# Performance work log

Measured on AMD Instinct MI355X. Metric: run time of the kernel, lower is better.

The kernel has to match this reference:

```python
import jax, jax.numpy as jnp
import numpy as np

B, T, R, E, H = 64, 512, 256, 512, 1024

def setup_inputs() -> dict:
    key = jax.random.key(0)
    ks = jax.random.split(key, 7)
    s = lambda d: 1.0 / np.sqrt(d)
    return {
        "x": jax.random.normal(ks[0], (B, T, R), jnp.float32),
        "W_emb": jax.random.normal(ks[1], (E, R), jnp.float32) * s(R),
        "b_emb": jax.random.normal(ks[2], (E,), jnp.float32) * s(R),
        "W_ih": jax.random.normal(ks[3], (4 * H, E), jnp.float32) * s(H),
        "W_hh": jax.random.normal(ks[4], (4 * H, H), jnp.float32) * s(H),
        "b_ih": jax.random.normal(ks[5], (4 * H,), jnp.float32) * s(H),
        "b_hh": jax.random.normal(ks[6], (4 * H,), jnp.float32) * s(H),
    }

def reference(x, W_emb, b_emb, W_ih, W_hh, b_ih, b_hh):
    # Per-timestep Linear embedding, batched over time (same math as the loop)
    xe = jnp.einsum('btr,er->bte', x, W_emb) + b_emb            # [B,T,E]
    # Input contribution to all gates, precomputed for every step
    gx = jnp.einsum('bte,ge->btg', xe, W_ih) + (b_ih + b_hh)    # [B,T,4H]

    def step(carry, gx_t):
        h, c = carry
        gates = gx_t + h @ W_hh.T                               # [B,4H]
        i, f, g, o = jnp.split(gates, 4, axis=-1)
        i = jax.nn.sigmoid(i)
        f = jax.nn.sigmoid(f)
        g = jnp.tanh(g)
        o = jax.nn.sigmoid(o)
        c_new = f * c + i * g
        h_new = o * jnp.tanh(c_new)
        return (h_new, c_new), h_new

    h0 = jnp.zeros((x.shape[0], H), x.dtype)
    c0 = jnp.zeros((x.shape[0], H), x.dtype)
    (h_t, c_t), ys = jax.lax.scan(step, (h0, c0), jnp.swapaxes(gx, 0, 1))
    outputs = jnp.swapaxes(ys, 0, 1)                            # [B,T,H]
    return outputs, h_t, c_t
```

## Files before the change

### kernel.cpp

```cpp
#include <hip/hip_runtime.h>
#include <stdint.h>

typedef __attribute__((ext_vector_type(8))) short short8;
typedef __attribute__((ext_vector_type(4))) float f32x4;
typedef __attribute__((ext_vector_type(4))) unsigned short ushort4v;
typedef unsigned long long u64;

__device__ inline unsigned short f2bf(float x) {
  union { float f; unsigned u; } v; v.f = x;
  unsigned r = (v.u + 0x7FFFu + ((v.u >> 16) & 1u)) >> 16;
  return (unsigned short)r;
}
__device__ inline float bf2f(unsigned short b) {
  union { unsigned u; float f; } v; v.u = ((unsigned)b) << 16;
  return v.f;
}
__device__ inline float fsig(float x) { return 1.f / (1.f + __expf(-x)); }

__device__ inline void gload_lds16(const void* g, void* l) {
  __builtin_amdgcn_global_load_lds(
      (const __attribute__((address_space(1))) unsigned int*)g,
      (__attribute__((address_space(3))) unsigned int*)l, 16, 0, 0);
}

__global__ void k_convert(const float* __restrict__ src, unsigned short* __restrict__ dst, int n4) {
  int i = blockIdx.x * blockDim.x + threadIdx.x;
  if (i < n4) {
    f32x4 v = *(const f32x4*)(src + (size_t)i * 4);
    ushort4v r;
    r.x = f2bf(v.x); r.y = f2bf(v.y); r.z = f2bf(v.z); r.w = f2bf(v.w);
    *(ushort4v*)(dst + (size_t)i * 4) = r;
  }
}

__global__ void k_bias(const float* __restrict__ a, const float* __restrict__ b,
                       float* __restrict__ o, int n) {
  int i = blockIdx.x * blockDim.x + threadIdx.x;
  if (i < n) o[i] = a[i] + b[i];
}

__global__ void k_init(unsigned short* __restrict__ h0, unsigned short* __restrict__ flags) {
  int i = blockIdx.x * blockDim.x + threadIdx.x;
  h0[i] = 0;
  if (i < 256) flags[i] = 0;
}

template <int MODE>
__global__ __launch_bounds__(256) void k_gemm_bt(
    const unsigned short* __restrict__ A,
    const unsigned short* __restrict__ Bm,
    const float* __restrict__ bias,
    unsigned short* __restrict__ C,
    int M, int N, int K) {
  __shared__ unsigned short As[128 * 32];
  __shared__ unsigned short Bs[128 * 32];
  const int tid = threadIdx.x;

  int bidx = blockIdx.x, bidy = blockIdx.y;
  if (MODE == 1) {
    int bid = blockIdx.y * gridDim.x + blockIdx.x;
    int cpx = (gridDim.x * gridDim.y) >> 3;
    int swz = (bid & 7) * cpx + (bid >> 3);
    bidy = swz / gridDim.x;
    bidx = swz % gridDim.x;
  }
  const int m0 = bidy * 128, n0 = bidx * 128;
  const int lane = tid & 63, w = tid >> 6;
  const int wm = (w >> 1) * 64, wn = (w & 1) * 64;

  f32x4 acc[4][4] = {};

  const int ar0 = tid >> 2;
  const int ak = (tid & 3) * 8;
  const unsigned short* Ag0 = A + (size_t)(m0 + ar0) * K + ak;
  const unsigned short* Ag1 = A + (size_t)(m0 + 64 + ar0) * K + ak;
  const unsigned short* Bg0 = Bm + (size_t)(n0 + ar0) * K + ak;
  const unsigned short* Bg1 = Bm + (size_t)(n0 + 64 + ar0) * K + ak;
  unsigned short* Al = As + tid * 8;
  unsigned short* Bl = Bs + tid * 8;

  const int lr = lane & 15, lk = (lane >> 4) * 8;

  for (int k0 = 0; k0 < K; k0 += 32) {
    gload_lds16(Ag0 + k0, Al);
    gload_lds16(Ag1 + k0, Al + 2048);
    gload_lds16(Bg0 + k0, Bl);
    gload_lds16(Bg1 + k0, Bl + 2048);
    __syncthreads();
    short8 a[4], b[4];
#pragma unroll
    for (int i = 0; i < 4; i++) a[i] = *(const short8*)&As[(wm + i * 16 + lr) * 32 + lk];
#pragma unroll
    for (int j = 0; j < 4; j++) b[j] = *(const short8*)&Bs[(wn + j * 16 + lr) * 32 + lk];
#pragma unroll
    for (int i = 0; i < 4; i++)
#pragma unroll
      for (int j = 0; j < 4; j++)
        acc[i][j] = __builtin_amdgcn_mfma_f32_16x16x32_bf16(a[i], b[j], acc[i][j], 0, 0, 0);
    __syncthreads();
  }

  const int lq = (lane >> 4) * 4;
#pragma unroll
  for (int j = 0; j < 4; j++) {
    int col = n0 + wn + j * 16 + lr;
    float bv = bias[col];
#pragma unroll
    for (int i = 0; i < 4; i++) {
      int rowb = m0 + wm + i * 16 + lq;
#pragma unroll
      for (int r = 0; r < 4; r++) {
        int row = rowb + r;
        float v = acc[i][j][r] + bv;
        if (MODE == 1) {
          int t = row & 511, bglob = row >> 9;
          int gg = bglob >> 4, bb = bglob & 15;
          int s = col >> 10, cc = col & 1023;
          int gtb = cc >> 4, cl = cc & 15;
          int wv = cl >> 2, qq = cl & 3;
          size_t idx = (size_t)t * 262144 + (size_t)gg * 65536 + (size_t)gtb * 1024
                     + (size_t)((wv * 64 + bb * 4 + qq) * 4 + s);
          C[idx] = f2bf(v);
        } else {
          C[(size_t)row * (size_t)N + col] = f2bf(v);
        }
      }
    }
  }
}

#define R32(F) F(0) F(1) F(2) F(3) F(4) F(5) F(6) F(7) \
               F(8) F(9) F(10) F(11) F(12) F(13) F(14) F(15) \
               F(16) F(17) F(18) F(19) F(20) F(21) F(22) F(23) \
               F(24) F(25) F(26) F(27) F(28) F(29) F(30) F(31)
#define WDECL(i) short8 w##i;
#define WLOAD(i) asm volatile("global_load_dwordx4 %0, %1, off offset:%c2" \
                              : "=v"(w##i) : "v"(wbase), "i"((i) * 64));
#define MFH(i, ACC) { \
    short8 a_ = *(const short8*)(HsB + lB + (i) * 1024); \
    ACC = __builtin_amdgcn_mfma_f32_16x16x32_bf16(a_, w##i, ACC, 0, 0, 0); }
#define MF2(i, ACC) { \
    union { u64 d[2]; short8 s; } u_; \
    u_.d[0] = __hip_atomic_load((const u64*)(hrow2 + (i) * 32), __ATOMIC_RELAXED, __HIP_MEMORY_SCOPE_AGENT); \
    u_.d[1] = __hip_atomic_load((const u64*)(hrow2 + (i) * 32 + 4), __ATOMIC_RELAXED, __HIP_MEMORY_SCOPE_AGENT); \
    ACC = __builtin_amdgcn_mfma_f32_16x16x32_bf16(u_.s, w##i, ACC, 0, 0, 0); }

template <int RING>
__global__ __launch_bounds__(256, 1) void k_persist(
    const unsigned short* __restrict__ gx3,
    const unsigned short* __restrict__ Whh,
    unsigned short* __restrict__ hring,
    unsigned short* __restrict__ flags,
    float* __restrict__ out,
    float* __restrict__ hout,
    float* __restrict__ cout) {
  __shared__ unsigned short Hs[16384];
  __shared__ float Gs[4][16 * 17 + 4];

  const int tid = threadIdx.x;
  const int g = blockIdx.x & 3, gt = blockIdx.x >> 2;
  const int lane = tid & 63, w = tid >> 6;
  const int lr = lane & 15, hi = lane >> 4;

  const int grow = (lr >> 2) * 1024 + gt * 16 + w * 4 + (lr & 3);
  const unsigned short* wbase = Whh + (size_t)grow * 1024 + hi * 8;
  R32(WDECL)
  R32(WLOAD)
  asm volatile("s_waitcnt vmcnt(0)" ::: "memory");
  __builtin_amdgcn_sched_barrier(0);

  const int cb = lane >> 2, cq = lane & 3;
  const int col = gt * 16 + w * 4 + cq;
  const int brow = g * 16 + cb;
  float c_reg = 0.f;

  const u64* gbase = (const u64*)gx3 + (size_t)g * 16384 + (size_t)gt * 256;
  u64 gv = gbase[tid];

  const char* HsB = (const char*)Hs;
  const int lB = hi * 256 + lr * 16;

  const u64* fpw = (const u64*)flags + g * 16 + w * 4 + (lane & 3);

  for (int t = 0; t < 512; ++t) {
    f32x4 ac0 = {}, ac1 = {}, ac2 = {}, ac3 = {};
    if (RING == 2) {
      if (w == 0) {
        const u64* fp = (const u64*)flags + g * 16 + lane;
        for (;;) {
          bool ok = true;
          if (lane < 16) {
            u64 f = __hip_atomic_load(fp, __ATOMIC_RELAXED, __HIP_MEMORY_SCOPE_AGENT);
            ok = ((int)(f & 0xFFFF) >= t) && ((int)((f >> 16) & 0xFFFF) >= t) &&
                 ((int)((f >> 32) & 0xFFFF) >= t) && ((int)(f >> 48) >= t);
          }
          if (__all(ok)) break;
        }
      }
      __syncthreads();
      __builtin_amdgcn_sched_barrier(0);
      const unsigned short* hrow2 = hring + (size_t)(t & 1) * 65536
                                  + (size_t)(g * 16 + lr) * 1024 + hi * 8;
      MF2(0, ac0)  MF2(1, ac1)  MF2(2, ac2)  MF2(3, ac3)
      MF2(4, ac0)  MF2(5, ac1)  MF2(6, ac2)  MF2(7, ac3)
      MF2(8, ac0)  MF2(9, ac1)  MF2(10, ac2) MF2(11, ac3)
      MF2(12, ac0) MF2(13, ac1) MF2(14, ac2) MF2(15, ac3)
      MF2(16, ac0) MF2(17, ac1) MF2(18, ac2) MF2(19, ac3)
      MF2(20, ac0) MF2(21, ac1) MF2(22, ac2) MF2(23, ac3)
      MF2(24, ac0) MF2(25, ac1) MF2(26, ac2) MF2(27, ac3)
      MF2(28, ac0) MF2(29, ac1) MF2(30, ac2) MF2(31, ac3)
    } else {
      for (;;) {
        u64 f = __hip_atomic_load(fpw, __ATOMIC_RELAXED, __HIP_MEMORY_SCOPE_AGENT);
        bool ok = ((int)(f & 0xFFFF) >= t) && ((int)((f >> 16) & 0xFFFF) >= t) &&
                  ((int)((f >> 32) & 0xFFFF) >= t) && ((int)(f >> 48) >= t);
        if (__all(ok)) break;
      }
      __builtin_amdgcn_sched_barrier(0);
      const unsigned short* hsrc = hring + (size_t)t * 65536 + (size_t)g * 16384;
#pragma unroll
      for (int i = 0; i < 8; ++i) {
        int ch = w * 512 + i * 64;
        gload_lds16(hsrc + ((size_t)ch + lane) * 8, Hs + (size_t)ch * 8);
      }
      asm volatile("s_waitcnt vmcnt(0)" ::: "memory");
      __builtin_amdgcn_sched_barrier(0);
      __syncthreads();
      MFH(0, ac0)  MFH(1, ac1)  MFH(2, ac2)  MFH(3, ac3)
      MFH(4, ac0)  MFH(5, ac1)  MFH(6, ac2)  MFH(7, ac3)
      MFH(8, ac0)  MFH(9, ac1)  MFH(10, ac2) MFH(11, ac3)
      MFH(12, ac0) MFH(13, ac1) MFH(14, ac2) MFH(15, ac3)
      MFH(16, ac0) MFH(17, ac1) MFH(18, ac2) MFH(19, ac3)
      MFH(20, ac0) MFH(21, ac1) MFH(22, ac2) MFH(23, ac3)
      MFH(24, ac0) MFH(25, ac1) MFH(26, ac2) MFH(27, ac3)
      MFH(28, ac0) MFH(29, ac1) MFH(30, ac2) MFH(31, ac3)
    }
    f32x4 accs = (ac0 + ac1) + (ac2 + ac3);

#pragma unroll
    for (int r = 0; r < 4; ++r)
      Gs[w][(hi * 4 + r) * 17 + lr] = accs[r];
    asm volatile("s_waitcnt lgkmcnt(0)" ::: "memory");
    __builtin_amdgcn_sched_barrier(0);

    float gi = Gs[w][cb * 17 + 0 + cq]  + bf2f((unsigned short)(gv));
    float gf = Gs[w][cb * 17 + 4 + cq]  + bf2f((unsigned short)(gv >> 16));
    float gg = Gs[w][cb * 17 + 8 + cq]  + bf2f((unsigned short)(gv >> 32));
    float go = Gs[w][cb * 17 + 12 + cq] + bf2f((unsigned short)(gv >> 48));
    float i_ = fsig(gi);
    float f_ = fsig(gf);
    float g_ = tanhf(gg);
    float o_ = fsig(go);
    float cn = f_ * c_reg + i_ * g_;
    float hn = o_ * tanhf(cn);
    c_reg = cn;

    if (t == 511) {
      __builtin_nontemporal_store(hn, &out[((size_t)brow * 512 + t) * 1024 + col]);
      hout[(size_t)brow * 1024 + col] = hn;
      cout[(size_t)brow * 1024 + col] = cn;
    } else {
      unsigned hu = f2bf(hn);
      unsigned v0 = __shfl(hu, (lane & ~3) + 0);
      unsigned v1 = __shfl(hu, (lane & ~3) + 1);
      unsigned v2 = __shfl(hu, (lane & ~3) + 2);
      unsigned v3 = __shfl(hu, (lane & ~3) + 3);
      if ((lane & 3) == 0) {
        u64 pack = (u64)(v0 & 0xFFFF) | ((u64)(v1 & 0xFFFF) << 16)
                 | ((u64)(v2 & 0xFFFF) << 32) | ((u64)(v3 & 0xFFFF) << 48);
        u64* hp;
        if (RING == 2) {
          hp = (u64*)(hring + (size_t)((t + 1) & 1) * 65536
                      + (size_t)brow * 1024 + gt * 16 + w * 4);
        } else {
          size_t e = (size_t)(gt * 2 + (w >> 1)) * 128 + (size_t)cb * 8 + (size_t)(w & 1) * 4;
          hp = (u64*)(hring + (size_t)(t + 1) * 65536 + (size_t)g * 16384 + e);
        }
        __hip_atomic_store(hp, pack, __ATOMIC_RELAXED, __HIP_MEMORY_SCOPE_AGENT);
      }
      __syncthreads();
      if (tid == 0)
        __hip_atomic_store(&flags[g * 64 + gt], (unsigned short)(t + 1),
                           __ATOMIC_RELAXED, __HIP_MEMORY_SCOPE_AGENT);
      __builtin_nontemporal_store(hn, &out[((size_t)brow * 512 + t) * 1024 + col]);
      gv = gbase[(size_t)(t + 1) * 65536 + tid];
    }
  }
}
#undef MF2
#undef MFH
#undef WLOAD
#undef WDECL
#undef R32

extern "C" void kernel_launch(void* const* d_in, const int* in_sizes, int n_in,
                              void* d_out, int out_size, void* d_ws, size_t ws_size,
                              hipStream_t stream) {
  const float* x = (const float*)d_in[0];
  const float* W_emb = (const float*)d_in[1];
  const float* b_emb = (const float*)d_in[2];
  const float* W_ih = (const float*)d_in[3];
  const float* W_hh = (const float*)d_in[4];
  const float* b_ih = (const float*)d_in[5];
  const float* b_hh = (const float*)d_in[6];

  char* ws = (char*)d_ws;
  unsigned short* x_bf    = (unsigned short*)(ws + 0);
  unsigned short* Wemb_bf = (unsigned short*)(ws + 16777216);
  unsigned short* Wih_bf  = (unsigned short*)(ws + 17039360);
  unsigned short* Whh_bf  = (unsigned short*)(ws + 21233664);
  float* bias_sum         = (float*)(ws + 29622272);
  unsigned short* xe      = (unsigned short*)(ws + 29638656);
  unsigned short* gx3     = (unsigned short*)(ws + 63193088);
  unsigned short* flags   = (unsigned short*)(ws + 331628544);
  unsigned short* hring   = (unsigned short*)(ws + 331632640);

  const size_t need_ring = 331632640ull + 512ull * 131072ull;
  const bool big = (ws_size >= need_ring);

  float* out = (float*)d_out;
  float* hout = out + (size_t)64 * 512 * 1024;
  float* cout = hout + 65536;

  k_convert<<<8192, 256, 0, stream>>>(x, x_bf, 2097152);
  k_convert<<<128, 256, 0, stream>>>(W_emb, Wemb_bf, 32768);
  k_convert<<<2048, 256, 0, stream>>>(W_ih, Wih_bf, 524288);
  k_convert<<<4096, 256, 0, stream>>>(W_hh, Whh_bf, 1048576);
  k_bias<<<16, 256, 0, stream>>>(b_ih, b_hh, bias_sum, 4096);
  k_init<<<256, 256, 0, stream>>>(hring, flags);

  k_gemm_bt<0><<<dim3(4, 256), 256, 0, stream>>>(x_bf, Wemb_bf, b_emb, xe, 32768, 512, 256);
  k_gemm_bt<1><<<dim3(32, 256), 256, 0, stream>>>(xe, Wih_bf, bias_sum, gx3, 32768, 4096, 512);

  if (big)
    k_persist<512><<<256, 256, 0, stream>>>(gx3, Whh_bf, hring, flags, out, hout, cout);
  else
    k_persist<2><<<256, 256, 0, stream>>>(gx3, Whh_bf, hring, flags, out, hout, cout);
}
```

Before: 2.144 ms.

## Fold embedding weights into input-gate weights to skip the xe GEMM

Precomputes W_comb = W_ih·W_emb (4096x256) and a combined bias W_ih·b_emb + b_ih + b_hh, so the gate pre-activations come from a single GEMM over x with K=256. This removes the large [B*T,512] embedding GEMM and its intermediate write/read, and halves K for the big gate GEMM. In exchange it adds a small weight-weight GEMM, a transpose kernel and a serial bias dot-product kernel. Rounding the combined weight to bf16 changes numerics slightly.

```diff
diff --git a/kernel.cpp b/kernel.cpp
--- a/kernel.cpp
+++ b/kernel.cpp
@@ -33,16 +33,27 @@
   }
 }
 
-__global__ void k_bias(const float* __restrict__ a, const float* __restrict__ b,
-                       float* __restrict__ o, int n) {
-  int i = blockIdx.x * blockDim.x + threadIdx.x;
-  if (i < n) o[i] = a[i] + b[i];
-}
-
-__global__ void k_init(unsigned short* __restrict__ h0, unsigned short* __restrict__ flags) {
+__global__ void k_temb(const float* __restrict__ We, unsigned short* __restrict__ WT) {
+  int o = blockIdx.x * blockDim.x + threadIdx.x;
+  int r = o >> 9, e = o & 511;
+  WT[o] = f2bf(We[e * 256 + r]);
+}
+
+__global__ void k_bcomb(const float* __restrict__ Wih, const float* __restrict__ b_emb,
+                        const float* __restrict__ b_ih, const float* __restrict__ b_hh,
+                        float* __restrict__ out) {
+  int g = blockIdx.x * blockDim.x + threadIdx.x;
+  const float* row = Wih + (size_t)g * 512;
+  float s = 0.f;
+  for (int e = 0; e < 512; ++e) s += row[e] * b_emb[e];
+  out[g] = s + b_ih[g] + b_hh[g];
+}
+
+__global__ void k_init(unsigned short* __restrict__ h0, unsigned short* __restrict__ flags,
+                       float* __restrict__ zerob) {
   int i = blockIdx.x * blockDim.x + threadIdx.x;
   h0[i] = 0;
-  if (i < 256) flags[i] = 0;
+  if (i < 256) { flags[i] = 0; zerob[i] = 0.f; }
 }
 
 template <int MODE>
@@ -306,11 +317,12 @@
 
   char* ws = (char*)d_ws;
   unsigned short* x_bf    = (unsigned short*)(ws + 0);
-  unsigned short* Wemb_bf = (unsigned short*)(ws + 16777216);
+  unsigned short* WembT   = (unsigned short*)(ws + 16777216);
   unsigned short* Wih_bf  = (unsigned short*)(ws + 17039360);
   unsigned short* Whh_bf  = (unsigned short*)(ws + 21233664);
-  float* bias_sum         = (float*)(ws + 29622272);
-  unsigned short* xe      = (unsigned short*)(ws + 29638656);
+  float* b_comb           = (float*)(ws + 29622272);
+  float* zerob            = (float*)(ws + 29638656);
+  unsigned short* Wcomb   = (unsigned short*)(ws + 29639680);
   unsigned short* gx3     = (unsigned short*)(ws + 63193088);
   unsigned short* flags   = (unsigned short*)(ws + 331628544);
   unsigned short* hring   = (unsigned short*)(ws + 331632640);
@@ -323,14 +335,14 @@
   float* cout = hout + 65536;
 
   k_convert<<<8192, 256, 0, stream>>>(x, x_bf, 2097152);
-  k_convert<<<128, 256, 0, stream>>>(W_emb, Wemb_bf, 32768);
   k_convert<<<2048, 256, 0, stream>>>(W_ih, Wih_bf, 524288);
   k_convert<<<4096, 256, 0, stream>>>(W_hh, Whh_bf, 1048576);
-  k_bias<<<16, 256, 0, stream>>>(b_ih, b_hh, bias_sum, 4096);
-  k_init<<<256, 256, 0, stream>>>(hring, flags);
-
-  k_gemm_bt<0><<<dim3(4, 256), 256, 0, stream>>>(x_bf, Wemb_bf, b_emb, xe, 32768, 512, 256);
-  k_gemm_bt<1><<<dim3(32, 256), 256, 0, stream>>>(xe, Wih_bf, bias_sum, gx3, 32768, 4096, 512);
+  k_temb<<<512, 256, 0, stream>>>(W_emb, WembT);
+  k_bcomb<<<16, 256, 0, stream>>>(W_ih, b_emb, b_ih, b_hh, b_comb);
+  k_init<<<256, 256, 0, stream>>>(hring, flags, zerob);
+
+  k_gemm_bt<0><<<dim3(2, 32), 256, 0, stream>>>(Wih_bf, WembT, zerob, Wcomb, 4096, 256, 512);
+  k_gemm_bt<1><<<dim3(32, 256), 256, 0, stream>>>(x_bf, Wcomb, b_comb, gx3, 32768, 4096, 256);
 
   if (big)
     k_persist<512><<<256, 256, 0, stream>>>(gx3, Whh_bf, hring, flags, out, hout, cout);
```

Measured after the change: 2.052 ms. 1.04x faster.
